# Performance work log

Hardware: AMD Instinct MI355X
Metric: run time of the kernel (lower is better)

The kernel has to match this reference:

```python
import jax, jax.numpy as jnp
import numpy as np


def setup_inputs() -> dict:
    key = jax.random.key(0)
    # x: [B, C, T, M] = [64, 4, 8192, 16]
    x = jax.random.normal(key, (64, 4, 8192, 16), dtype=jnp.float32)
    return {"x": x}


def reference(x) -> jnp.ndarray:
    # torch.cov(row[c].T): variables = last dim M, observations = T, correction=1.
    # Output: [B, C, M, M]
    T = x.shape[2]
    xc = x - jnp.mean(x, axis=2, keepdims=True)        # center over time axis
    cov = jnp.einsum('bctm,bctn->bcmn', xc, xc) / (T - 1)
    return cov
```

## Files before the change

### kernel.cpp

```cpp
#include <hip/hip_runtime.h>


constexpr int T_DIM = 8192;
constexpr int M_DIM = 16;
constexpr int BLOCK = 1024;
constexpr int NWAVE = BLOCK / 64;
constexpr int T_PER_WAVE = T_DIM / NWAVE;
constexpr int CHUNKS = T_PER_WAVE / 32;

using bf16x8 = __attribute__((ext_vector_type(8))) short;
using f32x4  = __attribute__((ext_vector_type(4))) float;

static __device__ inline short f2bf(float f) {
    union { float f; unsigned u; } v{f};
    unsigned r = v.u + 0x7fffu + ((v.u >> 16) & 1u);
    return (short)(r >> 16);
}

__global__ __launch_bounds__(BLOCK)
void cov_kernel(const float* __restrict__ x, float* __restrict__ out) {
    const int bc   = blockIdx.x;
    const int tid  = threadIdx.x;
    const int wave = tid >> 6;
    const int lane = tid & 63;
    const int q    = lane >> 4;
    const int m    = lane & 15;

    const int t0 = wave * T_PER_WAVE + q * 8;
    const float* __restrict__ base =
        x + (size_t)bc * (T_DIM * M_DIM) + (size_t)t0 * M_DIM + m;

    f32x4 acc = {0.f, 0.f, 0.f, 0.f};
    float sum = 0.f;

#pragma unroll 2
    for (int c = 0; c < CHUNKS; ++c) {
        const float* __restrict__ p = base + (size_t)c * 32 * M_DIM;
        float f0 = p[0 * M_DIM], f1 = p[1 * M_DIM];
        float f2 = p[2 * M_DIM], f3 = p[3 * M_DIM];
        float f4 = p[4 * M_DIM], f5 = p[5 * M_DIM];
        float f6 = p[6 * M_DIM], f7 = p[7 * M_DIM];
        sum += ((f0 + f1) + (f2 + f3)) + ((f4 + f5) + (f6 + f7));
        bf16x8 frag;
        frag[0] = f2bf(f0); frag[1] = f2bf(f1);
        frag[2] = f2bf(f2); frag[3] = f2bf(f3);
        frag[4] = f2bf(f4); frag[5] = f2bf(f5);
        frag[6] = f2bf(f6); frag[7] = f2bf(f7);
        acc = __builtin_amdgcn_mfma_f32_16x16x32_bf16(frag, frag, acc, 0, 0, 0);
    }

    sum += __shfl_xor(sum, 16, 64);
    sum += __shfl_xor(sum, 32, 64);

    __shared__ float Pred[NWAVE][256];
    __shared__ float Sred[NWAVE][M_DIM];
    __shared__ float Stot[M_DIM];

#pragma unroll
    for (int r = 0; r < 4; ++r)
        Pred[wave][(q * 4 + r) * M_DIM + m] = acc[r];
    if (lane < M_DIM) Sred[wave][lane] = sum;
    __syncthreads();

    if (tid < M_DIM) {
        float s = 0.f;
#pragma unroll
        for (int w = 0; w < NWAVE; ++w) s += Sred[w][tid];
        Stot[tid] = s;
    }
    __syncthreads();

    if (tid < 256) {
        float P = 0.f;
#pragma unroll
        for (int w = 0; w < NWAVE; ++w) P += Pred[w][tid];
        const int mi = tid >> 4;
        const int ni = tid & 15;
        const float cov = (P - Stot[mi] * Stot[ni] * (1.0f / (float)T_DIM))
                        * (1.0f / (float)(T_DIM - 1));
        out[(size_t)bc * 256 + tid] = cov;
    }
}

extern "C" void kernel_launch(void* const* d_in, const int* in_sizes, int n_in,
                              void* d_out, int out_size, void* d_ws, size_t ws_size,
                              hipStream_t stream) {
    const float* x = (const float*)d_in[0];
    float* out = (float*)d_out;
    const int n_bc = in_sizes[0] / (T_DIM * M_DIM);
    cov_kernel<<<dim3(n_bc), dim3(BLOCK), 0, stream>>>(x, out);
}
```

Before: 187.6 us.

## Load x with float4 vectors and transpose via LDS staging into MFMA fragments

Each lane now issues 16-byte float4 loads covering four features at two time steps. It packs pairs into bf16x2 words and writes them to a per-wave double-buffered, XOR-swizzled LDS stage, where each lane reads back its 8-element MFMA fragment. The loop also software-prefetches the next round's loads. The aim is to replace strided 4-byte scalar loads with wide coalesced loads, in exchange for extra LDS traffic and a shuffle-based column-sum reduction. There is no explicit barrier between the LDS write and read within a wave, so correctness relies on wave-level execution ordering.

```diff
diff --git a/kernel.cpp b/kernel.cpp
--- a/kernel.cpp
+++ b/kernel.cpp
@@ -6,15 +6,16 @@
 constexpr int BLOCK = 1024;
 constexpr int NWAVE = BLOCK / 64;
 constexpr int T_PER_WAVE = T_DIM / NWAVE;
-constexpr int CHUNKS = T_PER_WAVE / 32;
+constexpr int ROUNDS = T_PER_WAVE / 32;
 
 using bf16x8 = __attribute__((ext_vector_type(8))) short;
 using f32x4  = __attribute__((ext_vector_type(4))) float;
 
-static __device__ inline short f2bf(float f) {
-    union { float f; unsigned u; } v{f};
-    unsigned r = v.u + 0x7fffu + ((v.u >> 16) & 1u);
-    return (short)(r >> 16);
+static __device__ inline unsigned pack_bf2(float lo, float hi) {
+    union { float f; unsigned u; } a{lo}, b{hi};
+    unsigned ra = a.u + 0x7fffu + ((a.u >> 16) & 1u);
+    unsigned rb = b.u + 0x7fffu + ((b.u >> 16) & 1u);
+    return (ra >> 16) | (rb & 0xffff0000u);
 }
 
 __global__ __launch_bounds__(BLOCK)
@@ -23,43 +24,70 @@
     const int tid  = threadIdx.x;
     const int wave = tid >> 6;
     const int lane = tid & 63;
-    const int q    = lane >> 4;
-    const int m    = lane & 15;
 
-    const int t0 = wave * T_PER_WAVE + q * 8;
-    const float* __restrict__ base =
-        x + (size_t)bc * (T_DIM * M_DIM) + (size_t)t0 * M_DIM + m;
+    const int rg = lane & 15;
+    const int g  = lane >> 4;
+    const int q  = lane >> 4;
+    const int m  = lane & 15;
 
-    f32x4 acc = {0.f, 0.f, 0.f, 0.f};
-    float sum = 0.f;
-
-#pragma unroll 2
-    for (int c = 0; c < CHUNKS; ++c) {
-        const float* __restrict__ p = base + (size_t)c * 32 * M_DIM;
-        float f0 = p[0 * M_DIM], f1 = p[1 * M_DIM];
-        float f2 = p[2 * M_DIM], f3 = p[3 * M_DIM];
-        float f4 = p[4 * M_DIM], f5 = p[5 * M_DIM];
-        float f6 = p[6 * M_DIM], f7 = p[7 * M_DIM];
-        sum += ((f0 + f1) + (f2 + f3)) + ((f4 + f5) + (f6 + f7));
-        bf16x8 frag;
-        frag[0] = f2bf(f0); frag[1] = f2bf(f1);
-        frag[2] = f2bf(f2); frag[3] = f2bf(f3);
-        frag[4] = f2bf(f4); frag[5] = f2bf(f5);
-        frag[6] = f2bf(f6); frag[7] = f2bf(f7);
-        acc = __builtin_amdgcn_mfma_f32_16x16x32_bf16(frag, frag, acc, 0, 0, 0);
-    }
-
-    sum += __shfl_xor(sum, 16, 64);
-    sum += __shfl_xor(sum, 32, 64);
-
+    __shared__ __align__(16) unsigned stage[NWAVE][2][256];
     __shared__ float Pred[NWAVE][256];
     __shared__ float Sred[NWAVE][M_DIM];
     __shared__ float Stot[M_DIM];
 
+    const float4* __restrict__ xin =
+        (const float4*)(x + (size_t)bc * (T_DIM * M_DIM));
+
+    int idx = (wave * T_PER_WAVE + 2 * rg) * 4 + g;
+
+    const int qw = rg >> 2, dq = rg & 3;
+    const int roff = (q * 16 + (m ^ q)) * 4;
+
+    f32x4 acc = {0.f, 0.f, 0.f, 0.f};
+    float s0 = 0.f, s1 = 0.f, s2 = 0.f, s3 = 0.f;
+
+    float4 a0 = xin[idx], a1 = xin[idx + 4];
+
+#define COV_PROCESS(A0, A1, R)                                               \
+    do {                                                                     \
+        s0 += (A0).x + (A1).x;  s1 += (A0).y + (A1).y;                       \
+        s2 += (A0).z + (A1).z;  s3 += (A0).w + (A1).w;                       \
+        unsigned* wb = &stage[wave][(R) & 1][0];                             \
+        wb[(qw * 16 + ((4 * g + 0) ^ qw)) * 4 + dq] = pack_bf2((A0).x, (A1).x); \
+        wb[(qw * 16 + ((4 * g + 1) ^ qw)) * 4 + dq] = pack_bf2((A0).y, (A1).y); \
+        wb[(qw * 16 + ((4 * g + 2) ^ qw)) * 4 + dq] = pack_bf2((A0).z, (A1).z); \
+        wb[(qw * 16 + ((4 * g + 3) ^ qw)) * 4 + dq] = pack_bf2((A0).w, (A1).w); \
+        bf16x8 frag = *(const bf16x8*)&stage[wave][(R) & 1][roff];           \
+        acc = __builtin_amdgcn_mfma_f32_16x16x32_bf16(frag, frag, acc, 0, 0, 0); \
+    } while (0)
+
+#pragma unroll 4
+    for (int r = 0; r < ROUNDS - 1; ++r) {
+        const int nidx = idx + 32 * 4;
+        float4 b0 = xin[nidx], b1 = xin[nidx + 4];
+        COV_PROCESS(a0, a1, r);
+        a0 = b0; a1 = b1; idx = nidx;
+    }
+    COV_PROCESS(a0, a1, ROUNDS - 1);
+#undef COV_PROCESS
+
+#pragma unroll
+    for (int off = 1; off <= 8; off <<= 1) {
+        s0 += __shfl_xor(s0, off, 64);
+        s1 += __shfl_xor(s1, off, 64);
+        s2 += __shfl_xor(s2, off, 64);
+        s3 += __shfl_xor(s3, off, 64);
+    }
+    if (rg == 0) {
+        Sred[wave][4 * g + 0] = s0;
+        Sred[wave][4 * g + 1] = s1;
+        Sred[wave][4 * g + 2] = s2;
+        Sred[wave][4 * g + 3] = s3;
+    }
+
 #pragma unroll
     for (int r = 0; r < 4; ++r)
         Pred[wave][(q * 4 + r) * M_DIM + m] = acc[r];
-    if (lane < M_DIM) Sred[wave][lane] = sum;
     __syncthreads();
 
     if (tid < M_DIM) {
```

Result: no change. 185.3 us (-1.2%).
